# Kernel tuning notes

Measured on AMD Instinct MI355X. Metric: run time of the kernel, lower is better.

Reference implementation:

```python
import jax, jax.numpy as jnp
import numpy as np
from jax import lax

BN_EPS = 1e-5

def _maxpool_same(x, k):
    # x: [B, C, H, W]; stride-1 max pool with 'same' padding (pad value -inf, like torch)
    p = k // 2
    neg_inf = jnp.array(-jnp.inf, dtype=x.dtype)
    return lax.reduce_window(x, neg_inf, lax.max,
                             window_dimensions=(1, 1, k, k),
                             window_strides=(1, 1, 1, 1),
                             padding=[(0, 0), (0, 0), (p, p), (p, p)])

def setup_inputs() -> dict:
    key = jax.random.key(0)
    k1, k2 = jax.random.split(key)
    B, Cin, Cout, H, W_ = 16, 1024, 512, 32, 32
    x = jax.random.normal(k1, (B, Cin, H, W_), dtype=jnp.float32)
    W = jax.random.normal(k2, (Cout, Cin), dtype=jnp.float32) * (1.0 / np.sqrt(Cin))
    gamma = jnp.ones((Cout,), dtype=jnp.float32)
    beta = jnp.zeros((Cout,), dtype=jnp.float32)
    running_mean = jnp.zeros((Cout,), dtype=jnp.float32)
    running_var = jnp.ones((Cout,), dtype=jnp.float32)
    return {"x": x, "W": W, "gamma": gamma, "beta": beta,
            "running_mean": running_mean, "running_var": running_var}

def reference(x, W, gamma, beta, running_mean, running_var):
    # 1x1 conv (no bias): [B, Cin, H, W] x [Cout, Cin] -> [B, Cout, H, W]
    y = jnp.einsum('bchw,oc->bohw', x, W)
    # BatchNorm (inference form with running stats)
    inv = gamma * lax.rsqrt(running_var + BN_EPS)
    y = y * inv[None, :, None, None] + (beta - running_mean * inv)[None, :, None, None]
    # Mish activation
    y = y * jnp.tanh(jax.nn.softplus(y))
    # Three overlapping stride-1 max pools, concat channel-wise: [m13, m9, m5, y]
    return jnp.concatenate([_maxpool_same(y, 13), _maxpool_same(y, 9),
                            _maxpool_same(y, 5), y], axis=1)
```

## Files before the change

kernel.cpp:

```cpp
#include <hip/hip_runtime.h>
#include <hip/hip_bf16.h>
#include <math.h>

typedef __attribute__((ext_vector_type(4))) float  f32x4;
typedef __attribute__((ext_vector_type(8))) __bf16 bf16x8;
typedef __attribute__((ext_vector_type(4))) __bf16 bf16x4;

#define BN_EPS 1e-5f

__device__ __forceinline__ void gload16(const void* g, void* l) {
    __builtin_amdgcn_global_load_lds(
        (const __attribute__((address_space(1))) unsigned int*)g,
        (__attribute__((address_space(3))) unsigned int*)l, 16, 0, 0);
}

__global__ __launch_bounds__(256) void prep_transpose_kernel(
    const float* __restrict__ x, __bf16* __restrict__ xt,
    const float* __restrict__ W, const float* __restrict__ gamma,
    const float* __restrict__ beta, const float* __restrict__ rmean,
    const float* __restrict__ rvar, __bf16* __restrict__ Wb,
    float* __restrict__ sc, float* __restrict__ bs)
{
    __shared__ float lt[64][65];
    const int t = threadIdx.x;
    const int bid = blockIdx.x;

    if (bid >= 4096) {
        const int b2 = bid - 4096;
        const int t2 = b2 * 256 + t;
        const int idx = t2 * 4;
        f32x4 v = *(const f32x4*)(W + idx);
        bf16x4 o;
        o[0] = (__bf16)v[0]; o[1] = (__bf16)v[1];
        o[2] = (__bf16)v[2]; o[3] = (__bf16)v[3];
        *(bf16x4*)(Wb + idx) = o;
        if (b2 < 2) {
            int ch = b2 * 256 + t;
            float s = gamma[ch] * rsqrtf(rvar[ch] + BN_EPS);
            sc[ch] = s;
            bs[ch] = beta[ch] - rmean[ch] * s;
        }
        return;
    }

    const int b = bid >> 8;
    const int w = bid & 255;
    const int c0  = (w & 15) * 64;
    const int hw0 = (w >> 4) * 64;

    const int cl = t >> 4;
    const int q  = (t & 15) * 4;
    const float* src = x + (((size_t)(b * 1024 + c0 + cl)) << 10) + hw0 + q;
    #pragma unroll
    for (int i = 0; i < 4; ++i) {
        f32x4 v = *(const f32x4*)(src + ((size_t)i << 14));
        int c = cl + i * 16;
        lt[c][q + 0] = v[0]; lt[c][q + 1] = v[1];
        lt[c][q + 2] = v[2]; lt[c][q + 3] = v[3];
    }
    __syncthreads();

    const int hwl = t >> 3;
    const int oct = (t & 7) * 8;
    #pragma unroll
    for (int half = 0; half < 2; ++half) {
        const int hw = hwl + half * 32;
        bf16x8 v;
        #pragma unroll
        for (int i = 0; i < 8; ++i)
            v[i] = (__bf16)lt[oct + i][hw];
        *(bf16x8*)(xt + (((size_t)(b * 1024 + hw0 + hw)) << 10) + c0 + oct) = v;
    }
}

__global__ __launch_bounds__(256, 3) void gemm_kernel(
    const __bf16* __restrict__ Wb,
    const __bf16* __restrict__ xt,
    const float* __restrict__ sc, const float* __restrict__ bs,
    float* __restrict__ out)
{
    __shared__ __align__(16) char lds[32768];
    char* const Alds = lds;
    char* const Blds = lds + 16384;

    const int t  = threadIdx.x;
    const int f  = blockIdx.x + 4 * (blockIdx.y + 8 * blockIdx.z);
    const int f2 = (f & 7) * 64 + (f >> 3);
    const int o0  = (f2 & 3) * 128;
    const int hw0 = ((f2 >> 2) & 7) * 128;
    const int b   = f2 >> 5;

    const int srow = t >> 3;
    const int sswz = ((t & 7) ^ ((t >> 3) & 7)) * 16;
    const char* Ag = (const char*)Wb + (((size_t)(o0 + srow)) << 11) + sswz;
    const char* Bg = (const char*)xt + ((size_t)b << 21)
                   + (((size_t)(hw0 + srow)) << 11) + sswz;
    char* Al = Alds + t * 16;
    char* Bl = Blds + t * 16;

    const int l  = t & 63;
    const int lr = l & 15;
    const int lk = l >> 4;
    const int wm = (t >> 6) & 1;
    const int wn = t >> 7;

    int aoff[4][2], boff[4][2];
    #pragma unroll
    for (int i = 0; i < 4; ++i)
        #pragma unroll
        for (int kk = 0; kk < 2; ++kk) {
            int ra = wm * 64 + i * 16 + lr;
            int rb = wn * 64 + i * 16 + lr;
            int s  = lk + kk * 4;
            aoff[i][kk] = ra * 128 + ((s ^ (ra & 7)) * 16);
            boff[i][kk] = rb * 128 + ((s ^ (rb & 7)) * 16);
        }

    f32x4 acc[4][4] = {};

    for (int ks = 0; ks < 16; ++ks) {
        __syncthreads();
        const int kb = ks * 128;
        #pragma unroll
        for (int i = 0; i < 4; ++i) {
            gload16(Ag + (i << 16) + kb, Al + (i << 12));
            gload16(Bg + (i << 16) + kb, Bl + (i << 12));
        }
        __syncthreads();
        bf16x8 af[4][2], bfr[4][2];
        #pragma unroll
        for (int i = 0; i < 4; ++i)
            #pragma unroll
            for (int kk = 0; kk < 2; ++kk) {
                af[i][kk]  = *(const bf16x8*)(Alds + aoff[i][kk]);
                bfr[i][kk] = *(const bf16x8*)(Blds + boff[i][kk]);
            }
        #pragma unroll
        for (int kk = 0; kk < 2; ++kk)
            #pragma unroll
            for (int i = 0; i < 4; ++i)
                #pragma unroll
                for (int j = 0; j < 4; ++j)
                    acc[i][j] = __builtin_amdgcn_mfma_f32_16x16x32_bf16(
                        af[i][kk], bfr[j][kk], acc[i][j], 0, 0, 0);
    }

    const size_t outbase = (((size_t)b * 2048 + 1536) << 10);
    #pragma unroll
    for (int i = 0; i < 4; ++i) {
        const int ob = o0 + wm * 64 + i * 16 + lk * 4;
        const f32x4 s4 = *(const f32x4*)(sc + ob);
        const f32x4 b4 = *(const f32x4*)(bs + ob);
        #pragma unroll
        for (int r = 0; r < 4; ++r) {
            float* orow = out + outbase + (((size_t)(ob + r)) << 10)
                        + hw0 + wn * 64 + lr;
            #pragma unroll
            for (int j = 0; j < 4; ++j) {
                float v = acc[i][j][r] * s4[r] + b4[r];
                float e   = __expf(fminf(v, 15.0f));
                float num = e * (e + 2.0f);
                orow[j * 16] = v * (num / (num + 2.0f));
            }
        }
    }
}

__global__ __launch_bounds__(256) void pool_kernel(float* __restrict__ out)
{
    __shared__ float A[32][33];
    __shared__ float B[32][33];
    const int t = threadIdx.x;
    const int b = blockIdx.x >> 9;
    const int o = blockIdx.x & 511;
    const int r  = t >> 3;
    const int c0 = (t & 7) * 4;

    const size_t ybase = ((size_t)(b * 2048 + 1536 + o)) << 10;
    f32x4 v = *(const f32x4*)(out + ybase + t * 4);
    A[r][c0] = v[0]; A[r][c0 + 1] = v[1]; A[r][c0 + 2] = v[2]; A[r][c0 + 3] = v[3];
    __syncthreads();

    for (int p = 0; p < 3; ++p) {
        float wv[8];
        #pragma unroll
        for (int k = 0; k < 8; ++k) {
            int cc = c0 - 2 + k;
            wv[k] = (cc >= 0 && cc < 32) ? A[r][cc] : -INFINITY;
        }
        #pragma unroll
        for (int q = 0; q < 4; ++q) {
            float h = fmaxf(fmaxf(fmaxf(wv[q], wv[q + 1]), fmaxf(wv[q + 2], wv[q + 3])), wv[q + 4]);
            B[r][c0 + q] = h;
        }
        __syncthreads();
        f32x4 m;
        m[0] = m[1] = m[2] = m[3] = -INFINITY;
        #pragma unroll
        for (int k = 0; k < 5; ++k) {
            int rr = r - 2 + k;
            if (rr >= 0 && rr < 32) {
                m[0] = fmaxf(m[0], B[rr][c0]);
                m[1] = fmaxf(m[1], B[rr][c0 + 1]);
                m[2] = fmaxf(m[2], B[rr][c0 + 2]);
                m[3] = fmaxf(m[3], B[rr][c0 + 3]);
            }
        }
        A[r][c0] = m[0]; A[r][c0 + 1] = m[1]; A[r][c0 + 2] = m[2]; A[r][c0 + 3] = m[3];
        const size_t obase = ((size_t)(b * 2048 + (2 - p) * 512 + o)) << 10;
        *(f32x4*)(out + obase + t * 4) = m;
        __syncthreads();
    }
}

extern "C" void kernel_launch(void* const* d_in, const int* in_sizes, int n_in,
                              void* d_out, int out_size, void* d_ws, size_t ws_size,
                              hipStream_t stream)
{
    const float* x     = (const float*)d_in[0];
    const float* W     = (const float*)d_in[1];
    const float* gamma = (const float*)d_in[2];
    const float* beta  = (const float*)d_in[3];
    const float* rmean = (const float*)d_in[4];
    const float* rvar  = (const float*)d_in[5];
    float* out = (float*)d_out;
    char*  ws  = (char*)d_ws;

    __bf16* xt = (__bf16*)ws;
    __bf16* Wb = (__bf16*)(ws + 33554432);
    float*  sc = (float*)(ws + 34603008);
    float*  bs = (float*)(ws + 34605056);

    prep_transpose_kernel<<<4608, 256, 0, stream>>>(x, xt, W, gamma, beta, rmean, rvar, Wb, sc, bs);
    gemm_kernel<<<dim3(4, 8, 16), 256, 0, stream>>>(Wb, xt, sc, bs, out);
    pool_kernel<<<8192, 256, 0, stream>>>(out);
}
```

Before: 69.90 us.

## Fuse GEMM, BN-Mish and cascaded max pools into one LDS-resident kernel

Merges the 1x1-conv GEMM and the pooling kernel into a single kernel. Each 512-thread block computes a 32-output-channel by full-spatial tile for one batch, keeps the Mish outputs in a 128KB LDS buffer, and runs the cascaded 5x5 pools from LDS. This removes the global round trip of y between the two kernels and one launch. In exchange the GEMM tiles become much smaller (32x128 per step with one accumulator pair per wave), occupancy drops to one block per CU, and only 256 blocks are launched, so MFMA efficiency and latency hiding may suffer.

```diff
diff --git a/kernel.cpp b/kernel.cpp
--- a/kernel.cpp
+++ b/kernel.cpp
@@ -5,6 +5,7 @@
 typedef __attribute__((ext_vector_type(4))) float  f32x4;
 typedef __attribute__((ext_vector_type(8))) __bf16 bf16x8;
 typedef __attribute__((ext_vector_type(4))) __bf16 bf16x4;
+typedef __attribute__((ext_vector_type(2))) __bf16 bf16x2;
 
 #define BN_EPS 1e-5f
 
@@ -73,143 +74,140 @@
     }
 }
 
-__global__ __launch_bounds__(256, 3) void gemm_kernel(
+__global__ __launch_bounds__(512, 1) void spp_kernel(
     const __bf16* __restrict__ Wb,
     const __bf16* __restrict__ xt,
     const float* __restrict__ sc, const float* __restrict__ bs,
     float* __restrict__ out)
 {
-    __shared__ __align__(16) char lds[32768];
-    char* const Alds = lds;
-    char* const Blds = lds + 16384;
+    __shared__ __align__(16) char smem[151552];
+    float* const yl  = (float*)smem;
+    char*  const Alds = smem + 131072;
+    char*  const Blds = smem + 135168;
 
     const int t  = threadIdx.x;
-    const int f  = blockIdx.x + 4 * (blockIdx.y + 8 * blockIdx.z);
-    const int f2 = (f & 7) * 64 + (f >> 3);
-    const int o0  = (f2 & 3) * 128;
-    const int hw0 = ((f2 >> 2) & 7) * 128;
-    const int b   = f2 >> 5;
-
-    const int srow = t >> 3;
-    const int sswz = ((t & 7) ^ ((t >> 3) & 7)) * 16;
-    const char* Ag = (const char*)Wb + (((size_t)(o0 + srow)) << 11) + sswz;
-    const char* Bg = (const char*)xt + ((size_t)b << 21)
-                   + (((size_t)(hw0 + srow)) << 11) + sswz;
-    char* Al = Alds + t * 16;
-    char* Bl = Blds + t * 16;
+    const int id = blockIdx.x;
+    const int xcd = id & 7, j = id >> 3;
+    const int b  = xcd + 8 * (j >> 4);
+    const int ob = j & 15;
+
+    const char* Agb = (const char*)Wb + ((size_t)(ob * 32) << 11);
+    const char* Bgb = (const char*)xt + ((size_t)b << 21);
+    const int offA  = (t >> 3) * 2048 + ((((t) & 7) ^ ((t >> 3) & 7)) << 4);
+    const int s2 = t + 512;
+    const int offB0 = (t  >> 3) * 2048 + (((t  & 7) ^ ((t  >> 3) & 7)) << 4);
+    const int offB1 = (s2 >> 3) * 2048 + (((s2 & 7) ^ ((s2 >> 3) & 7)) << 4);
 
     const int l  = t & 63;
     const int lr = l & 15;
     const int lk = l >> 4;
-    const int wm = (t >> 6) & 1;
-    const int wn = t >> 7;
-
-    int aoff[4][2], boff[4][2];
-    #pragma unroll
-    for (int i = 0; i < 4; ++i)
+    const int wv = t >> 6;
+
+    int aoff[2][2], boff[2];
+    #pragma unroll
+    for (int i = 0; i < 2; ++i)
         #pragma unroll
         for (int kk = 0; kk < 2; ++kk) {
-            int ra = wm * 64 + i * 16 + lr;
-            int rb = wn * 64 + i * 16 + lr;
+            int ra = i * 16 + lr;
             int s  = lk + kk * 4;
-            aoff[i][kk] = ra * 128 + ((s ^ (ra & 7)) * 16);
-            boff[i][kk] = rb * 128 + ((s ^ (rb & 7)) * 16);
-        }
-
-    f32x4 acc[4][4] = {};
-
-    for (int ks = 0; ks < 16; ++ks) {
-        __syncthreads();
-        const int kb = ks * 128;
+            aoff[i][kk] = ra * 128 + ((s ^ (ra & 7)) << 4);
+        }
+    #pragma unroll
+    for (int kk = 0; kk < 2; ++kk) {
+        int rb = wv * 16 + lr;
+        boff[kk] = rb * 128 + (((lk + kk * 4) ^ (rb & 7)) << 4);
+    }
+
+    f32x4 s4[2], b4[2];
+    #pragma unroll
+    for (int i = 0; i < 2; ++i) {
+        s4[i] = *(const f32x4*)(sc + ob * 32 + i * 16 + lk * 4);
+        b4[i] = *(const f32x4*)(bs + ob * 32 + i * 16 + lk * 4);
+    }
+
+    for (int sub = 0; sub < 8; ++sub) {
+        const int hw0s = sub * 128;
+        const char* Bsub = Bgb + ((size_t)hw0s << 11);
+        f32x4 acc[2] = {};
+        for (int ks = 0; ks < 16; ++ks) {
+            __syncthreads();
+            const int kb = ks * 128;
+            if (t < 256)
+                gload16(Agb + offA + kb, Alds + t * 16);
+            gload16(Bsub + offB0 + kb, Blds + t * 16);
+            gload16(Bsub + offB1 + kb, Blds + s2 * 16);
+            __syncthreads();
+            bf16x8 af[2][2], bfv[2];
+            #pragma unroll
+            for (int i = 0; i < 2; ++i)
+                #pragma unroll
+                for (int kk = 0; kk < 2; ++kk)
+                    af[i][kk] = *(const bf16x8*)(Alds + aoff[i][kk]);
+            #pragma unroll
+            for (int kk = 0; kk < 2; ++kk)
+                bfv[kk] = *(const bf16x8*)(Blds + boff[kk]);
+            #pragma unroll
+            for (int kk = 0; kk < 2; ++kk)
+                #pragma unroll
+                for (int i = 0; i < 2; ++i)
+                    acc[i] = __builtin_amdgcn_mfma_f32_16x16x32_bf16(
+                        af[i][kk], bfv[kk], acc[i], 0, 0, 0);
+        }
+        const int hwp = hw0s + wv * 16 + lr;
         #pragma unroll
-        for (int i = 0; i < 4; ++i) {
-            gload16(Ag + (i << 16) + kb, Al + (i << 12));
-            gload16(Bg + (i << 16) + kb, Bl + (i << 12));
-        }
-        __syncthreads();
-        bf16x8 af[4][2], bfr[4][2];
-        #pragma unroll
-        for (int i = 0; i < 4; ++i)
-            #pragma unroll
-            for (int kk = 0; kk < 2; ++kk) {
-                af[i][kk]  = *(const bf16x8*)(Alds + aoff[i][kk]);
-                bfr[i][kk] = *(const bf16x8*)(Blds + boff[i][kk]);
-            }
-        #pragma unroll
-        for (int kk = 0; kk < 2; ++kk)
-            #pragma unroll
-            for (int i = 0; i < 4; ++i)
-                #pragma unroll
-                for (int j = 0; j < 4; ++j)
-                    acc[i][j] = __builtin_amdgcn_mfma_f32_16x16x32_bf16(
-                        af[i][kk], bfr[j][kk], acc[i][j], 0, 0, 0);
-    }
-
-    const size_t outbase = (((size_t)b * 2048 + 1536) << 10);
-    #pragma unroll
-    for (int i = 0; i < 4; ++i) {
-        const int ob = o0 + wm * 64 + i * 16 + lk * 4;
-        const f32x4 s4 = *(const f32x4*)(sc + ob);
-        const f32x4 b4 = *(const f32x4*)(bs + ob);
-        #pragma unroll
-        for (int r = 0; r < 4; ++r) {
-            float* orow = out + outbase + (((size_t)(ob + r)) << 10)
-                        + hw0 + wn * 64 + lr;
-            #pragma unroll
-            for (int j = 0; j < 4; ++j) {
-                float v = acc[i][j][r] * s4[r] + b4[r];
+        for (int i = 0; i < 2; ++i) {
+            #pragma unroll
+            for (int r = 0; r < 4; ++r) {
+                float v = acc[i][r] * s4[i][r] + b4[i][r];
                 float e   = __expf(fminf(v, 15.0f));
                 float num = e * (e + 2.0f);
-                orow[j * 16] = v * (num / (num + 2.0f));
+                float m = v * (num / (num + 2.0f));
+                const int ol = i * 16 + lk * 4 + r;
+                out[(((size_t)(b * 2048 + 1536 + ob * 32 + ol)) << 10) + hwp] = m;
+                yl[ol * 1024 + hwp] = m;
             }
         }
     }
-}
-
-__global__ __launch_bounds__(256) void pool_kernel(float* __restrict__ out)
-{
-    __shared__ float A[32][33];
-    __shared__ float B[32][33];
-    const int t = threadIdx.x;
-    const int b = blockIdx.x >> 9;
-    const int o = blockIdx.x & 511;
-    const int r  = t >> 3;
-    const int c0 = (t & 7) * 4;
-
-    const size_t ybase = ((size_t)(b * 2048 + 1536 + o)) << 10;
-    f32x4 v = *(const f32x4*)(out + ybase + t * 4);
-    A[r][c0] = v[0]; A[r][c0 + 1] = v[1]; A[r][c0 + 2] = v[2]; A[r][c0 + 3] = v[3];
     __syncthreads();
 
-    for (int p = 0; p < 3; ++p) {
-        float wv[8];
-        #pragma unroll
-        for (int k = 0; k < 8; ++k) {
-            int cc = c0 - 2 + k;
-            wv[k] = (cc >= 0 && cc < 32) ? A[r][cc] : -INFINITY;
-        }
-        #pragma unroll
-        for (int q = 0; q < 4; ++q) {
-            float h = fmaxf(fmaxf(fmaxf(wv[q], wv[q + 1]), fmaxf(wv[q + 2], wv[q + 3])), wv[q + 4]);
-            B[r][c0 + q] = h;
-        }
-        __syncthreads();
-        f32x4 m;
-        m[0] = m[1] = m[2] = m[3] = -INFINITY;
-        #pragma unroll
-        for (int k = 0; k < 5; ++k) {
-            int rr = r - 2 + k;
-            if (rr >= 0 && rr < 32) {
-                m[0] = fmaxf(m[0], B[rr][c0]);
-                m[1] = fmaxf(m[1], B[rr][c0 + 1]);
-                m[2] = fmaxf(m[2], B[rr][c0 + 2]);
-                m[3] = fmaxf(m[3], B[rr][c0 + 3]);
+    float* const Btmp = (float*)(smem + 131072);
+    const int tt = t & 255, hf = t >> 8;
+    const int r  = tt >> 3;
+    const int c0 = (tt & 7) * 4;
+    float* const Bt = Btmp + hf * 1056;
+
+    for (int it = 0; it < 16; ++it) {
+        const int ch = it * 2 + hf;
+        float* const yc = yl + ch * 1024;
+        for (int p = 0; p < 3; ++p) {
+            float w8[8];
+            #pragma unroll
+            for (int k = 0; k < 8; ++k) {
+                int cc = c0 - 2 + k;
+                w8[k] = (cc >= 0 && cc < 32) ? yc[r * 32 + cc] : -INFINITY;
             }
-        }
-        A[r][c0] = m[0]; A[r][c0 + 1] = m[1]; A[r][c0 + 2] = m[2]; A[r][c0 + 3] = m[3];
-        const size_t obase = ((size_t)(b * 2048 + (2 - p) * 512 + o)) << 10;
-        *(f32x4*)(out + obase + t * 4) = m;
-        __syncthreads();
+            #pragma unroll
+            for (int q = 0; q < 4; ++q)
+                Bt[r * 33 + c0 + q] =
+                    fmaxf(fmaxf(fmaxf(w8[q], w8[q + 1]), fmaxf(w8[q + 2], w8[q + 3])), w8[q + 4]);
+            __syncthreads();
+            f32x4 m;
+            m[0] = m[1] = m[2] = m[3] = -INFINITY;
+            #pragma unroll
+            for (int k = 0; k < 5; ++k) {
+                int rr = r - 2 + k;
+                if (rr >= 0 && rr < 32) {
+                    m[0] = fmaxf(m[0], Bt[rr * 33 + c0]);
+                    m[1] = fmaxf(m[1], Bt[rr * 33 + c0 + 1]);
+                    m[2] = fmaxf(m[2], Bt[rr * 33 + c0 + 2]);
+                    m[3] = fmaxf(m[3], Bt[rr * 33 + c0 + 3]);
+                }
+            }
+            *(f32x4*)(yc + r * 32 + c0) = m;
+            *(f32x4*)(out + (((size_t)(b * 2048 + (2 - p) * 512 + ob * 32 + ch)) << 10)
+                      + r * 32 + c0) = m;
+            __syncthreads();
+        }
     }
 }
 
@@ -232,6 +230,5 @@
     float*  bs = (float*)(ws + 34605056);
 
     prep_transpose_kernel<<<4608, 256, 0, stream>>>(x, xt, W, gamma, beta, rmean, rvar, Wb, sc, bs);
-    gemm_kernel<<<dim3(4, 8, 16), 256, 0, stream>>>(Wb, xt, sc, bs, out);
-    pool_kernel<<<8192, 256, 0, stream>>>(out);
-}
+    spp_kernel<<<256, 512, 0, stream>>>(Wb, xt, sc, bs, out);
+}
```

After: 133.2 us. 90.6% more time.
